# Kernel tuning notes

Hardware: AMD Instinct MI355X
Metric: run time of the kernel (lower is better)

## Reference

```python
import jax, jax.numpy as jnp
import numpy as np

NUM_HEADS = 16

def setup_inputs() -> dict:
    key = jax.random.key(0)
    ks = jax.random.split(key, 6)
    C = 512
    nW, B, N = 64, 4, 144
    x = jax.random.normal(ks[0], (B * nW, N, C), dtype=jnp.float32)
    mask = jax.random.randint(ks[1], (nW, N, N), 0, 2, dtype=jnp.int32)
    Wqkv = jax.random.normal(ks[2], (C, 3 * C), dtype=jnp.float32) * (1.0 / np.sqrt(C))
    bqkv = jnp.zeros((3 * C,), dtype=jnp.float32)
    Wproj = jax.random.normal(ks[3], (C, C), dtype=jnp.float32) * (1.0 / np.sqrt(C))
    bproj = jnp.zeros((C,), dtype=jnp.float32)
    return {"x": x, "mask": mask, "Wqkv": Wqkv, "bqkv": bqkv, "Wproj": Wproj, "bproj": bproj}

def reference(x, mask, Wqkv, bqkv, Wproj, bproj):
    Bn, N, C = x.shape
    H = NUM_HEADS
    D = C // H
    nW = mask.shape[0]
    B = Bn // nW
    scale = 1.0 / jnp.sqrt(jnp.asarray(D, dtype=x.dtype))

    qkv = x @ Wqkv + bqkv                        # (Bn, N, 3C)
    qkv = qkv.reshape(Bn, N, 3, H, D)            # packed order (qkv, H, D)
    qkv = jnp.transpose(qkv, (2, 0, 3, 1, 4))    # (3, Bn, H, N, D)
    q, k, v = qkv[0], qkv[1], qkv[2]

    # split window-batch dim: (B nW) -> B, nW
    q = q.reshape(B, nW, H, N, D)
    k = k.reshape(B, nW, H, N, D)
    v = v.reshape(B, nW, H, N, D)

    attn = jnp.einsum('bwhnd,bwhmd->bwhnm', q, k) * scale
    bias = jnp.where(mask == 0, -jnp.inf, 0.0).astype(x.dtype)  # (nW, N, N)
    attn = attn + bias.reshape(1, nW, 1, N, N)
    attn = jax.nn.softmax(attn, axis=-1)

    out = jnp.einsum('bwhnm,bwhmd->bwhnd', attn, v)   # (B, nW, H, N, D)
    out = jnp.transpose(out, (0, 1, 3, 2, 4)).reshape(Bn, N, C)
    return out @ Wproj + bproj
```

## Files before the change

kernel.cpp:

```cpp
#include <hip/hip_runtime.h>

typedef unsigned short u16;
typedef unsigned int u32;
typedef __attribute__((ext_vector_type(4))) float f32x4;
typedef __attribute__((ext_vector_type(8))) short bf16x8;
typedef __attribute__((ext_vector_type(4))) u32 u32x4;

__device__ __forceinline__ u16 f2bf(float f) {
  union { float f; u32 u; } v; v.f = f;
  u32 r = v.u + 0x7fffu + ((v.u >> 16) & 1u);
  return (u16)(r >> 16);
}

__device__ __forceinline__ void gload_lds16(const u16* g, u16* l) {
  __builtin_amdgcn_global_load_lds((__attribute__((address_space(1))) const void*)g,
                                   (__attribute__((address_space(3))) void*)l,
                                   16, 0, 0);
}

__global__ void __launch_bounds__(256) k_transpose_w(const float* __restrict__ W,
                                                     u16* __restrict__ Wt, int K, int Nc) {
  __shared__ u16 t[64][72];
  const int tid = threadIdx.x;
  const int kb = blockIdx.x * 64, nb = blockIdx.y * 64;
  const int c4 = (tid & 15) * 4;
  const int r0 = tid >> 4;
#pragma unroll
  for (int rr = 0; rr < 4; ++rr) {
    int r = rr * 16 + r0;
    float4 v = *(const float4*)(W + (size_t)(kb + r) * Nc + nb + c4);
    t[r][c4 + 0] = f2bf(v.x);
    t[r][c4 + 1] = f2bf(v.y);
    t[r][c4 + 2] = f2bf(v.z);
    t[r][c4 + 3] = f2bf(v.w);
  }
  __syncthreads();
  const int c8 = (tid & 7) * 8;
  const int rn = tid >> 3;
#pragma unroll
  for (int rr = 0; rr < 2; ++rr) {
    int n = rr * 32 + rn;
    u16 tmp[8];
#pragma unroll
    for (int j = 0; j < 8; ++j) tmp[j] = t[c8 + j][n];
    *(u32x4*)(Wt + (size_t)(nb + n) * K + kb + c8) = *(const u32x4*)tmp;
  }
}

__global__ void k_mask_bits(const int* __restrict__ mask, u32* __restrict__ mtab) {
  int idx = blockIdx.x * blockDim.x + threadIdx.x;
  if (idx >= 64 * 144 * 8) return;
  int wd = idx & 7;
  int r = idx >> 3;
  u32 bits = 0;
  if (wd < 5) {
    int base = r * 144 + wd * 32;
    int nmax = 144 - wd * 32;
    if (nmax > 32) nmax = 32;
    for (int b = 0; b < nmax; ++b) bits |= (mask[base + b] ? 1u : 0u) << b;
  }
  mtab[idx] = bits;
}

template <bool OUT_BF16, bool A_FP32>
__global__ void __launch_bounds__(256) k_gemm(const void* __restrict__ Ap,
                                              const u16* __restrict__ Bt,
                                              const float* __restrict__ bias,
                                              void* __restrict__ D,
                                              int Nc, int K, int NB) {
  __shared__ u16 As[128 * 64];
  __shared__ u16 Bs[128 * 64];
  const int tid = threadIdx.x;
  const int wave = tid >> 6, lane = tid & 63;
  const int wr = wave >> 1, wc = wave & 1;
  const int l15 = lane & 15, g = lane >> 4;
  const int sx = l15 & 7;
  const f32x4 fzero = {0.f, 0.f, 0.f, 0.f};

  const int cpx = gridDim.x >> 3;
  const int swz = (blockIdx.x & 7) * cpx + (blockIdx.x >> 3);
  const int bm = swz / NB, bn = swz % NB;

  const u16* Bb = Bt + (size_t)bn * 128 * K;

  f32x4 acc[4][4];
#pragma unroll
  for (int m = 0; m < 4; ++m)
#pragma unroll
    for (int n = 0; n < 4; ++n) acc[m][n] = fzero;

  const int nt = K >> 6;

  f32x4 areg[4][2];

  auto A_LOAD = [&](int t) {
    if constexpr (A_FP32) {
      const float* Af = (const float*)Ap;
#pragma unroll
      for (int i = 0; i < 4; ++i) {
        int e = i * 256 + tid;
        int r = e >> 3, c = e & 7;
        int cs = c ^ (r & 7);
        const float* p = Af + (size_t)(bm * 128 + r) * K + (t << 6) + cs * 8;
        areg[i][0] = *(const f32x4*)(p);
        areg[i][1] = *(const f32x4*)(p + 4);
      }
    }
  };

  auto A_WRITE = [&]() {
    if constexpr (A_FP32) {
#pragma unroll
      for (int i = 0; i < 4; ++i) {
        int e = i * 256 + tid;
        u32 w0, w1, w2, w3;
        asm("v_cvt_pk_bf16_f32 %0, %1, %2" : "=v"(w0) : "v"(areg[i][0][0]), "v"(areg[i][0][1]));
        asm("v_cvt_pk_bf16_f32 %0, %1, %2" : "=v"(w1) : "v"(areg[i][0][2]), "v"(areg[i][0][3]));
        asm("v_cvt_pk_bf16_f32 %0, %1, %2" : "=v"(w2) : "v"(areg[i][1][0]), "v"(areg[i][1][1]));
        asm("v_cvt_pk_bf16_f32 %0, %1, %2" : "=v"(w3) : "v"(areg[i][1][2]), "v"(areg[i][1][3]));
        u32x4 wv = {w0, w1, w2, w3};
        *(u32x4*)(&As[e * 8]) = wv;
      }
    }
  };

  auto A_STAGE_G = [&](int t) {
    if constexpr (!A_FP32) {
      const u16* Ab = (const u16*)Ap + (size_t)bm * 128 * K;
#pragma unroll
      for (int i = 0; i < 4; ++i) {
        int e = i * 256 + tid;
        int r = e >> 3, c = e & 7;
        int cs = c ^ (r & 7);
        gload_lds16(Ab + (size_t)r * K + (t << 6) + (cs << 3), &As[e * 8]);
      }
    }
  };

  auto B_STAGE = [&](int t) {
#pragma unroll
    for (int i = 0; i < 4; ++i) {
      int e = i * 256 + tid;
      int r = e >> 3, c = e & 7;
      int cs = c ^ (r & 7);
      gload_lds16(Bb + (size_t)r * K + (t << 6) + (cs << 3), &Bs[e * 8]);
    }
  };

  auto COMPUTE = [&]() {
#pragma unroll
    for (int kk = 0; kk < 2; ++kk) {
      const int cx = ((kk * 4 + g) ^ sx) << 3;
      bf16x8 a[4], b[4];
#pragma unroll
      for (int m = 0; m < 4; ++m)
        a[m] = *(const bf16x8*)(&As[(wr * 64 + m * 16 + l15) * 64 + cx]);
#pragma unroll
      for (int n = 0; n < 4; ++n)
        b[n] = *(const bf16x8*)(&Bs[(wc * 64 + n * 16 + l15) * 64 + cx]);
#pragma unroll
      for (int m = 0; m < 4; ++m)
#pragma unroll
        for (int n = 0; n < 4; ++n)
          acc[m][n] = __builtin_amdgcn_mfma_f32_16x16x32_bf16(a[m], b[n], acc[m][n], 0, 0, 0);
    }
  };

  if constexpr (A_FP32) {
    A_LOAD(0);
    for (int t = 0; t < nt; ++t) {
      A_WRITE();
      B_STAGE(t);
      if (t + 1 < nt) {
        A_LOAD(t + 1);
        asm volatile("s_waitcnt vmcnt(8) lgkmcnt(0)" ::: "memory");
      } else {
        asm volatile("s_waitcnt vmcnt(0) lgkmcnt(0)" ::: "memory");
      }
      __builtin_amdgcn_sched_barrier(0);
      __builtin_amdgcn_s_barrier();
      __builtin_amdgcn_sched_barrier(0);
      COMPUTE();
      __builtin_amdgcn_sched_barrier(0);
      __builtin_amdgcn_s_barrier();
    }
  } else {
    for (int t = 0; t < nt; ++t) {
      A_STAGE_G(t);
      B_STAGE(t);
      asm volatile("s_waitcnt vmcnt(0)" ::: "memory");
      __builtin_amdgcn_sched_barrier(0);
      __builtin_amdgcn_s_barrier();
      __builtin_amdgcn_sched_barrier(0);
      COMPUTE();
      __builtin_amdgcn_sched_barrier(0);
      __builtin_amdgcn_s_barrier();
    }
  }

  const int row0 = bm * 128 + wr * 64;
  const int col0 = bn * 128 + wc * 64;
#pragma unroll
  for (int m = 0; m < 4; ++m) {
#pragma unroll
    for (int n = 0; n < 4; ++n) {
      int col = col0 + n * 16 + l15;
      float bv = bias[col];
#pragma unroll
      for (int j = 0; j < 4; ++j) {
        int row = row0 + m * 16 + g * 4 + j;
        float v = acc[m][n][j] + bv;
        if constexpr (OUT_BF16)
          ((u16*)D)[(size_t)row * Nc + col] = f2bf(v);
        else
          ((float*)D)[(size_t)row * Nc + col] = v;
      }
    }
  }
}

__global__ void __launch_bounds__(256) k_attn(const u16* __restrict__ qkv,
                                              const u32* __restrict__ mtab,
                                              u16* __restrict__ obuf) {
  __shared__ u16 k_s[144 * 40];
  __shared__ u16 vT_s[32 * 168];
  __shared__ u16 P_s[4][16 * 168];

  const int bh = blockIdx.x;
  const int bn = bh >> 4, h = bh & 15;
  const int wid = bn & 63;
  const int tid = threadIdx.x;
  const int wave = tid >> 6, lane = tid & 63;
  const int l15 = lane & 15, g = lane >> 4;
  const f32x4 fzero = {0.f, 0.f, 0.f, 0.f};

  const u16* base = qkv + (size_t)bn * 144 * 1536 + h * 32;

  for (int e = tid; e < 576; e += 256) {
    int n = e >> 2, c = e & 3;
    const u16* rowp = base + (size_t)n * 1536 + c * 8;
    u32x4 kv = *(const u32x4*)(rowp + 512);
    u32x4 vv = *(const u32x4*)(rowp + 1024);
    *(u32x4*)(k_s + n * 40 + c * 8) = kv;
#pragma unroll
    for (int t = 0; t < 4; ++t) {
      u32 w = vv[t];
      vT_s[(c * 8 + 2 * t) * 168 + n] = (u16)(w & 0xffffu);
      vT_s[(c * 8 + 2 * t + 1) * 168 + n] = (u16)(w >> 16);
    }
  }
  for (int e = tid; e < 512; e += 256) {
    int d = e >> 4, c = e & 15;
    vT_s[d * 168 + 144 + c] = 0;
  }
  __syncthreads();

  const float scale = 0.17677669529663687f;
  u16* Pw = &P_s[wave][0];

  for (int mt = wave; mt < 9; mt += 4) {
    u32 mw[4][5];
#pragma unroll
    for (int j = 0; j < 4; ++j) {
      int r = mt * 16 + g * 4 + j;
      const u32* mp = mtab + ((size_t)(wid * 144 + r) << 3);
#pragma unroll
      for (int wd = 0; wd < 5; ++wd) mw[j][wd] = mp[wd];
    }

    bf16x8 a = *(const bf16x8*)(base + (size_t)(mt * 16 + l15) * 1536 + g * 8);

    f32x4 accs[9];
#pragma unroll
    for (int nt = 0; nt < 9; ++nt) {
      bf16x8 b = *(const bf16x8*)(k_s + (nt * 16 + l15) * 40 + g * 8);
      accs[nt] = __builtin_amdgcn_mfma_f32_16x16x32_bf16(a, b, fzero, 0, 0, 0);
    }

    float rmax[4] = {-1e30f, -1e30f, -1e30f, -1e30f};
#pragma unroll
    for (int nt = 0; nt < 9; ++nt) {
      const int wd = nt >> 1;
      const int sh = (nt & 1) * 16;
#pragma unroll
      for (int j = 0; j < 4; ++j) {
        float x = accs[nt][j] * scale;
        u32 bit = (mw[j][wd] >> (sh + l15)) & 1u;
        x = bit ? x : -1e9f;
        accs[nt][j] = x;
        rmax[j] = fmaxf(rmax[j], x);
      }
    }
#pragma unroll
    for (int off = 1; off < 16; off <<= 1)
#pragma unroll
      for (int j = 0; j < 4; ++j)
        rmax[j] = fmaxf(rmax[j], __shfl_xor(rmax[j], off, 64));

    float rsum[4] = {0.f, 0.f, 0.f, 0.f};
#pragma unroll
    for (int nt = 0; nt < 9; ++nt)
#pragma unroll
      for (int j = 0; j < 4; ++j) {
        float p = __expf(accs[nt][j] - rmax[j]);
        accs[nt][j] = p;
        rsum[j] += p;
      }
#pragma unroll
    for (int off = 1; off < 16; off <<= 1)
#pragma unroll
      for (int j = 0; j < 4; ++j)
        rsum[j] += __shfl_xor(rsum[j], off, 64);
    float rinv[4];
#pragma unroll
    for (int j = 0; j < 4; ++j) rinv[j] = 1.f / rsum[j];

#pragma unroll
    for (int nt = 0; nt < 9; ++nt)
#pragma unroll
      for (int j = 0; j < 4; ++j)
        Pw[(g * 4 + j) * 168 + nt * 16 + l15] = f2bf(accs[nt][j] * rinv[j]);
#pragma unroll
    for (int j = 0; j < 4; ++j)
      Pw[(g * 4 + j) * 168 + 144 + l15] = 0;

    asm volatile("s_waitcnt lgkmcnt(0)" ::: "memory");
    __builtin_amdgcn_sched_barrier(0);

    f32x4 acco[2];
    acco[0] = fzero;
    acco[1] = fzero;
#pragma unroll
    for (int kk = 0; kk < 5; ++kk) {
      bf16x8 pa = *(const bf16x8*)(Pw + l15 * 168 + kk * 32 + g * 8);
#pragma unroll
      for (int nt2 = 0; nt2 < 2; ++nt2) {
        bf16x8 b = *(const bf16x8*)(vT_s + (nt2 * 16 + l15) * 168 + kk * 32 + g * 8);
        acco[nt2] = __builtin_amdgcn_mfma_f32_16x16x32_bf16(pa, b, acco[nt2], 0, 0, 0);
      }
    }
#pragma unroll
    for (int nt2 = 0; nt2 < 2; ++nt2)
#pragma unroll
      for (int j = 0; j < 4; ++j) {
        int r = mt * 16 + g * 4 + j;
        int d = nt2 * 16 + l15;
        obuf[((size_t)bn * 144 + r) * 512 + h * 32 + d] = f2bf(acco[nt2][j]);
      }
  }
}

extern "C" void kernel_launch(void* const* d_in, const int* in_sizes, int n_in,
                              void* d_out, int out_size, void* d_ws, size_t ws_size,
                              hipStream_t stream) {
  const float* x = (const float*)d_in[0];
  const int* mask = (const int*)d_in[1];
  const float* Wqkv = (const float*)d_in[2];
  const float* bqkv = (const float*)d_in[3];
  const float* Wproj = (const float*)d_in[4];
  const float* bproj = (const float*)d_in[5];
  float* out = (float*)d_out;

  char* ws = (char*)d_ws;
  u32* mtab    = (u32*)(ws + 0);
  u16* wqkv_t  = (u16*)(ws + 294912);
  u16* qkv     = (u16*)(ws + 1867776);
  u16* obuf    = (u16*)(ws + 115113984);
  u16* wproj_t = (u16*)(ws + 152862720);

  k_transpose_w<<<dim3(8, 24), 256, 0, stream>>>(Wqkv, wqkv_t, 512, 1536);
  k_transpose_w<<<dim3(8, 8), 256, 0, stream>>>(Wproj, wproj_t, 512, 512);
  k_mask_bits<<<288, 256, 0, stream>>>(mask, mtab);
  k_gemm<true, true><<<3456, 256, 0, stream>>>(x, wqkv_t, bqkv, qkv, 1536, 512, 12);
  k_attn<<<4096, 256, 0, stream>>>(qkv, mtab, obuf);
  k_gemm<false, false><<<1152, 256, 0, stream>>>(obuf, wproj_t, bproj, out, 512, 512, 4);
}
```

Before: 223.8 us.

## Double-buffer B tile in LDS and stage A through registers with padded layout

The GEMM mainloop is restructured so the next B tile is fetched asynchronously into a second LDS buffer while the current tile is computed. A is now always loaded into registers one step ahead, for both fp32 and bf16 inputs, and written into a padded (stride 68) LDS tile instead of an XOR-swizzled one. Launch bounds request 3 blocks per CU. The aim is to overlap global loads with MFMA work and drop one barrier per iteration, at the cost of more LDS use and 16-byte LDS accesses on a stride that is only 8-byte aligned, which may split or conflict.

After: 220.6 us. Within noise of the previous version (-1.4%).

```diff
diff --git a/kernel.cpp b/kernel.cpp
--- a/kernel.cpp
+++ b/kernel.cpp
@@ -63,13 +63,13 @@
 }
 
 template <bool OUT_BF16, bool A_FP32>
-__global__ void __launch_bounds__(256) k_gemm(const void* __restrict__ Ap,
-                                              const u16* __restrict__ Bt,
-                                              const float* __restrict__ bias,
-                                              void* __restrict__ D,
-                                              int Nc, int K, int NB) {
-  __shared__ u16 As[128 * 64];
-  __shared__ u16 Bs[128 * 64];
+__global__ void __launch_bounds__(256, 3) k_gemm(const void* __restrict__ Ap,
+                                                 const u16* __restrict__ Bt,
+                                                 const float* __restrict__ bias,
+                                                 void* __restrict__ D,
+                                                 int Nc, int K, int NB) {
+  __shared__ u16 As[128 * 68];
+  __shared__ u16 Bs[2][128 * 64];
   const int tid = threadIdx.x;
   const int wave = tid >> 6, lane = tid & 63;
   const int wr = wave >> 1, wc = wave & 1;
@@ -83,81 +83,76 @@
 
   const u16* Bb = Bt + (size_t)bn * 128 * K;
 
+  int rr[4], cc[4];
+#pragma unroll
+  for (int i = 0; i < 4; ++i) {
+    int e = i * 256 + tid;
+    rr[i] = e >> 3;
+    cc[i] = e & 7;
+  }
+
   f32x4 acc[4][4];
 #pragma unroll
   for (int m = 0; m < 4; ++m)
 #pragma unroll
     for (int n = 0; n < 4; ++n) acc[m][n] = fzero;
 
-  const int nt = K >> 6;
-
-  f32x4 areg[4][2];
-
-  auto A_LOAD = [&](int t) {
+  f32x4 areg[8];
+  u32x4 aregb[4];
+
+  auto A_LOAD = [&](int ks) {
     if constexpr (A_FP32) {
       const float* Af = (const float*)Ap;
 #pragma unroll
       for (int i = 0; i < 4; ++i) {
-        int e = i * 256 + tid;
-        int r = e >> 3, c = e & 7;
-        int cs = c ^ (r & 7);
-        const float* p = Af + (size_t)(bm * 128 + r) * K + (t << 6) + cs * 8;
-        areg[i][0] = *(const f32x4*)(p);
-        areg[i][1] = *(const f32x4*)(p + 4);
-      }
+        const float* p = Af + (size_t)(bm * 128 + rr[i]) * K + ks + cc[i] * 8;
+        areg[2 * i] = *(const f32x4*)(p);
+        areg[2 * i + 1] = *(const f32x4*)(p + 4);
+      }
+    } else {
+      const u16* Ab = (const u16*)Ap + (size_t)bm * 128 * K;
+#pragma unroll
+      for (int i = 0; i < 4; ++i)
+        aregb[i] = *(const u32x4*)(Ab + (size_t)rr[i] * K + ks + cc[i] * 8);
     }
   };
 
   auto A_WRITE = [&]() {
-    if constexpr (A_FP32) {
-#pragma unroll
-      for (int i = 0; i < 4; ++i) {
-        int e = i * 256 + tid;
+#pragma unroll
+    for (int i = 0; i < 4; ++i) {
+      u32x4 wv;
+      if constexpr (A_FP32) {
         u32 w0, w1, w2, w3;
-        asm("v_cvt_pk_bf16_f32 %0, %1, %2" : "=v"(w0) : "v"(areg[i][0][0]), "v"(areg[i][0][1]));
-        asm("v_cvt_pk_bf16_f32 %0, %1, %2" : "=v"(w1) : "v"(areg[i][0][2]), "v"(areg[i][0][3]));
-        asm("v_cvt_pk_bf16_f32 %0, %1, %2" : "=v"(w2) : "v"(areg[i][1][0]), "v"(areg[i][1][1]));
-        asm("v_cvt_pk_bf16_f32 %0, %1, %2" : "=v"(w3) : "v"(areg[i][1][2]), "v"(areg[i][1][3]));
-        u32x4 wv = {w0, w1, w2, w3};
-        *(u32x4*)(&As[e * 8]) = wv;
-      }
+        asm("v_cvt_pk_bf16_f32 %0, %1, %2" : "=v"(w0) : "v"(areg[2 * i][0]), "v"(areg[2 * i][1]));
+        asm("v_cvt_pk_bf16_f32 %0, %1, %2" : "=v"(w1) : "v"(areg[2 * i][2]), "v"(areg[2 * i][3]));
+        asm("v_cvt_pk_bf16_f32 %0, %1, %2" : "=v"(w2) : "v"(areg[2 * i + 1][0]), "v"(areg[2 * i + 1][1]));
+        asm("v_cvt_pk_bf16_f32 %0, %1, %2" : "=v"(w3) : "v"(areg[2 * i + 1][2]), "v"(areg[2 * i + 1][3]));
+        wv[0] = w0; wv[1] = w1; wv[2] = w2; wv[3] = w3;
+      } else {
+        wv = aregb[i];
+      }
+      *(u32x4*)(&As[rr[i] * 68 + cc[i] * 8]) = wv;
     }
   };
 
-  auto A_STAGE_G = [&](int t) {
-    if constexpr (!A_FP32) {
-      const u16* Ab = (const u16*)Ap + (size_t)bm * 128 * K;
-#pragma unroll
-      for (int i = 0; i < 4; ++i) {
-        int e = i * 256 + tid;
-        int r = e >> 3, c = e & 7;
-        int cs = c ^ (r & 7);
-        gload_lds16(Ab + (size_t)r * K + (t << 6) + (cs << 3), &As[e * 8]);
-      }
+  auto B_STAGE = [&](int buf, int ks) {
+#pragma unroll
+    for (int i = 0; i < 4; ++i) {
+      int cs = cc[i] ^ (rr[i] & 7);
+      gload_lds16(Bb + (size_t)rr[i] * K + ks + (cs << 3), &Bs[buf][(i * 256 + tid) * 8]);
     }
   };
 
-  auto B_STAGE = [&](int t) {
-#pragma unroll
-    for (int i = 0; i < 4; ++i) {
-      int e = i * 256 + tid;
-      int r = e >> 3, c = e & 7;
-      int cs = c ^ (r & 7);
-      gload_lds16(Bb + (size_t)r * K + (t << 6) + (cs << 3), &Bs[e * 8]);
-    }
-  };
-
-  auto COMPUTE = [&]() {
+  auto COMPUTE = [&](int buf) {
 #pragma unroll
     for (int kk = 0; kk < 2; ++kk) {
-      const int cx = ((kk * 4 + g) ^ sx) << 3;
       bf16x8 a[4], b[4];
 #pragma unroll
       for (int m = 0; m < 4; ++m)
-        a[m] = *(const bf16x8*)(&As[(wr * 64 + m * 16 + l15) * 64 + cx]);
+        a[m] = *(const bf16x8*)(&As[(wr * 64 + m * 16 + l15) * 68 + (kk * 4 + g) * 8]);
 #pragma unroll
       for (int n = 0; n < 4; ++n)
-        b[n] = *(const bf16x8*)(&Bs[(wc * 64 + n * 16 + l15) * 64 + cx]);
+        b[n] = *(const bf16x8*)(&Bs[buf][(wc * 64 + n * 16 + l15) * 64 + (((kk * 4 + g) ^ sx) << 3)]);
 #pragma unroll
       for (int m = 0; m < 4; ++m)
 #pragma unroll
@@ -166,36 +161,24 @@
     }
   };
 
-  if constexpr (A_FP32) {
-    A_LOAD(0);
-    for (int t = 0; t < nt; ++t) {
-      A_WRITE();
-      B_STAGE(t);
-      if (t + 1 < nt) {
-        A_LOAD(t + 1);
-        asm volatile("s_waitcnt vmcnt(8) lgkmcnt(0)" ::: "memory");
-      } else {
-        asm volatile("s_waitcnt vmcnt(0) lgkmcnt(0)" ::: "memory");
-      }
-      __builtin_amdgcn_sched_barrier(0);
-      __builtin_amdgcn_s_barrier();
-      __builtin_amdgcn_sched_barrier(0);
-      COMPUTE();
-      __builtin_amdgcn_sched_barrier(0);
-      __builtin_amdgcn_s_barrier();
-    }
-  } else {
-    for (int t = 0; t < nt; ++t) {
-      A_STAGE_G(t);
-      B_STAGE(t);
-      asm volatile("s_waitcnt vmcnt(0)" ::: "memory");
-      __builtin_amdgcn_sched_barrier(0);
-      __builtin_amdgcn_s_barrier();
-      __builtin_amdgcn_sched_barrier(0);
-      COMPUTE();
-      __builtin_amdgcn_sched_barrier(0);
-      __builtin_amdgcn_s_barrier();
-    }
+  const int nt = K >> 6;
+  A_LOAD(0);
+  B_STAGE(0, 0);
+  int cur = 0;
+  for (int t = 0; t < nt; ++t) {
+    asm volatile("s_waitcnt vmcnt(0)" ::: "memory");
+    __builtin_amdgcn_sched_barrier(0);
+    if (t + 1 < nt) B_STAGE(cur ^ 1, (t + 1) << 6);
+    A_WRITE();
+    if (t + 1 < nt) A_LOAD((t + 1) << 6);
+    asm volatile("s_waitcnt lgkmcnt(0)" ::: "memory");
+    __builtin_amdgcn_sched_barrier(0);
+    __builtin_amdgcn_s_barrier();
+    __builtin_amdgcn_sched_barrier(0);
+    COMPUTE(cur);
+    __builtin_amdgcn_sched_barrier(0);
+    if (t + 1 < nt) __builtin_amdgcn_s_barrier();
+    cur ^= 1;
   }
 
   const int row0 = bm * 128 + wr * 64;
```
